# Performance work log

Measured on AMD Instinct MI355X. Metric: run time of the kernel, lower is better.

The kernel has to match this reference:

```python
import jax, jax.numpy as jnp
import numpy as np

EPS = 1e-5

@jax.custom_vjp
def binarize(x):
    # sign quantization: {-1, +1} (0 -> +1), as in BinaryNet Binarize
    return jnp.where(x >= 0, 1.0, -1.0).astype(x.dtype)

def _bin_fwd(x):
    return binarize(x), x

def _bin_bwd(res, g):
    # straight-through estimator with hardtanh clipping
    return (g * (jnp.abs(res) <= 1.0).astype(g.dtype),)

binarize.defvjp(_bin_fwd, _bin_bwd)


def batchnorm(x, gamma, beta):
    # BatchNorm1d, training mode: biased batch statistics over the batch axis
    mu = jnp.mean(x, axis=0)
    var = jnp.var(x, axis=0)
    return (x - mu) * jax.lax.rsqrt(var + EPS) * gamma + beta


def setup_inputs() -> dict:
    key = jax.random.key(0)
    ks = jax.random.split(key, 5)
    B, IND, HID, OUT = 16384, 768, 4096, 10
    return {
        "x": jax.random.normal(ks[0], (B, 784), jnp.float32),
        "w1": jax.random.normal(ks[1], (HID, IND), jnp.float32) * 0.05,
        "w2": jax.random.normal(ks[2], (HID, HID), jnp.float32) * 0.05,
        "w3": jax.random.normal(ks[3], (HID, HID), jnp.float32) * 0.05,
        "w4": jax.random.normal(ks[4], (OUT, HID), jnp.float32) * 0.05,
        "g1": jnp.ones(HID, jnp.float32), "b1": jnp.zeros(HID, jnp.float32),
        "g2": jnp.ones(HID, jnp.float32), "b2": jnp.zeros(HID, jnp.float32),
        "g3": jnp.ones(HID, jnp.float32), "b3": jnp.zeros(HID, jnp.float32),
        "g4": jnp.ones(OUT, jnp.float32), "b4": jnp.zeros(OUT, jnp.float32),
    }


def reference(x, w1, w2, w3, w4, g1, b1, g2, b2, g3, b3, g4, b4):
    # x.view(-1, 784); if width == 784, keep first 768 features
    h = x.reshape(-1, 784)[:, :768]
    # BinarizeLinear: binarize activations (width != 784) and weights, then matmul
    h = binarize(h) @ binarize(w1).T            # [B, 4096]
    h = jnp.clip(batchnorm(h, g1, b1), -1.0, 1.0)  # bn1 + hardtanh1
    h = binarize(h) @ binarize(w2).T
    h = jnp.clip(batchnorm(h, g2, b2), -1.0, 1.0)
    h = binarize(h) @ binarize(w3).T
    h = jnp.clip(batchnorm(h, g3, b3), -1.0, 1.0)
    h = binarize(h) @ binarize(w4).T            # [B, 10]
    h = batchnorm(h, g4, b4)
    return jax.nn.log_softmax(h, axis=1)
```

## Files before the change

### kernel.cpp

```cpp
#include <hip/hip_runtime.h>
#include <hip/hip_bf16.h>
#include <stdint.h>

typedef int v4i __attribute__((ext_vector_type(4)));

#define DEVI static __device__ __forceinline__

DEVI void gload16(const void* g, void* l) {
    __builtin_amdgcn_global_load_lds(
        (const __attribute__((address_space(1))) void*)g,
        (__attribute__((address_space(3))) void*)l,
        16, 0, 0);
}

#define WAITV(n) asm volatile("s_waitcnt vmcnt(" #n ")" ::: "memory")
#define SBAR()   __builtin_amdgcn_s_barrier()

__global__ __launch_bounds__(256) void k_bin_f32_to_i8(
    const float* __restrict__ w, int8_t* __restrict__ o, int n16)
{
    int t = blockIdx.x * 256 + threadIdx.x;
    if (t >= n16) return;
    const float4* s = (const float4*)w + (size_t)t * 4;
    union { int4 v; int8_t b[16]; } u;
#pragma unroll
    for (int i = 0; i < 4; ++i) {
        float4 f = s[i];
        u.b[i*4+0] = (f.x >= 0.f) ? (int8_t)1 : (int8_t)-1;
        u.b[i*4+1] = (f.y >= 0.f) ? (int8_t)1 : (int8_t)-1;
        u.b[i*4+2] = (f.z >= 0.f) ? (int8_t)1 : (int8_t)-1;
        u.b[i*4+3] = (f.w >= 0.f) ? (int8_t)1 : (int8_t)-1;
    }
    *(int4*)(o + (size_t)t * 16) = u.v;
}

__global__ __launch_bounds__(256) void k_bin_x(
    const float* __restrict__ x, int8_t* __restrict__ o)
{
    int t = blockIdx.x * 256 + threadIdx.x;
    int row = t / 48;
    int ch  = t % 48;
    const float4* s = (const float4*)(x + (size_t)row * 784 + ch * 16);
    union { int4 v; int8_t b[16]; } u;
#pragma unroll
    for (int i = 0; i < 4; ++i) {
        float4 f = s[i];
        u.b[i*4+0] = (f.x >= 0.f) ? (int8_t)1 : (int8_t)-1;
        u.b[i*4+1] = (f.y >= 0.f) ? (int8_t)1 : (int8_t)-1;
        u.b[i*4+2] = (f.z >= 0.f) ? (int8_t)1 : (int8_t)-1;
        u.b[i*4+3] = (f.w >= 0.f) ? (int8_t)1 : (int8_t)-1;
    }
    *(int4*)(o + (size_t)row * 768 + ch * 16) = u.v;
}

__global__ __launch_bounds__(512, 2)
void k_gemm256(const int8_t* __restrict__ A, const int8_t* __restrict__ B,
               int16_t* __restrict__ C, int* __restrict__ gsum,
               unsigned long long* __restrict__ gsq,
               int N, int K, int nbx)
{
    __shared__ __align__(16) int8_t lds[131072];

    const int tid  = threadIdx.x;
    const int lane = tid & 63;
    const int wave = tid >> 6;

    const int cpx = gridDim.x >> 3;
    const int id  = blockIdx.x;
    const int sw  = (id & 7) * cpx + (id >> 3);
    const int bx  = sw % nbx;
    const int by  = sw / nbx;

    const int NT = K >> 6;

    const int sr  = tid >> 2;
    const int asw = (((tid & 3) ^ ((sr >> 1) & 3)) << 4);
    const int8_t* gA0 = A + (size_t)(by * 256 + sr)       * K + asw;
    const int8_t* gA1 = A + (size_t)(by * 256 + 128 + sr) * K + asw;
    const int8_t* gB0 = B + (size_t)(bx * 256 + sr)       * K + asw;
    const int8_t* gB1 = B + (size_t)(bx * 256 + 128 + sr) * K + asw;
    const int ld0 = (wave * 64) << 4;
    const int ld1 = (512 + wave * 64) << 4;

    const int lrow = lane & 15;
    const int ksl  = lane >> 4;
    const int wr = (wave >> 2) * 128;
    const int wc = (wave & 3) * 64;
    const int fsw = ((ksl ^ ((lrow >> 1) & 3)) << 4);
    int aoff[8], boff[4];
#pragma unroll
    for (int m = 0; m < 8; ++m) aoff[m] = ((wr + m * 16 + lrow) << 6) + fsw;
#pragma unroll
    for (int n = 0; n < 4; ++n) boff[n] = ((wc + n * 16 + lrow) << 6) + fsw;

    v4i acc[8][4];
    v4i zero = {0, 0, 0, 0};
#pragma unroll
    for (int m = 0; m < 8; ++m)
#pragma unroll
        for (int n = 0; n < 4; ++n) acc[m][n] = zero;

#define STAGE_A(kt) do { const int _o = (kt) << 6; const int _b = ((kt) & 3) * 16384; \
        gload16(gA0 + _o, lds + _b + ld0); gload16(gA1 + _o, lds + _b + ld1); } while (0)
#define STAGE_B(kt) do { const int _o = (kt) << 6; const int _b = ((kt) & 3) * 16384; \
        gload16(gB0 + _o, lds + 65536 + _b + ld0); gload16(gB1 + _o, lds + 65536 + _b + ld1); } while (0)

#define READF(da, db, slot) do {                                                  \
        const int8_t* _ab = lds + ((slot) * 16384);                               \
        const int8_t* _bb = lds + 65536 + ((slot) * 16384);                       \
        _Pragma("unroll") for (int m = 0; m < 4; ++m)                             \
            da[m] = *(const v4i*)(_ab + aoff[m]);                                 \
        _Pragma("unroll") for (int n = 0; n < 4; ++n)                             \
            db[n] = *(const v4i*)(_bb + boff[n]); } while (0)

#define TILEF(kt, CA, CB, NA, NB) do {                                            \
        const int8_t* _ab = lds + (((kt) & 3) * 16384);                           \
        if ((kt) + 3 < NT) STAGE_A((kt) + 3);                                     \
        v4i _ag[4];                                                               \
        _Pragma("unroll") for (int m = 0; m < 4; ++m)                             \
            _ag[m] = *(const v4i*)(_ab + aoff[4 + m]);                            \
        SBAR();                                                                   \
        __builtin_amdgcn_s_setprio(1);                                            \
        _Pragma("unroll") for (int m = 0; m < 4; ++m)                             \
        _Pragma("unroll") for (int n = 0; n < 4; ++n)                             \
            acc[m][n] = __builtin_amdgcn_mfma_i32_16x16x64_i8(                    \
                CA[m], CB[n], acc[m][n], 0, 0, 0);                                \
        __builtin_amdgcn_s_setprio(0);                                            \
        SBAR();                                                                   \
        if ((kt) + 3 < NT) STAGE_B((kt) + 3);                                     \
        if ((kt) < NT - 3)       { WAITV(4); }                                    \
        else if ((kt) == NT - 3) { WAITV(0); }                                    \
        READF(NA, NB, ((kt) + 1) & 3);                                            \
        SBAR();                                                                   \
        __builtin_amdgcn_s_setprio(1);                                            \
        _Pragma("unroll") for (int m = 0; m < 4; ++m)                             \
        _Pragma("unroll") for (int n = 0; n < 4; ++n)                             \
            acc[4 + m][n] = __builtin_amdgcn_mfma_i32_16x16x64_i8(                \
                _ag[m], CB[n], acc[4 + m][n], 0, 0, 0);                           \
        __builtin_amdgcn_s_setprio(0);                                            \
        SBAR(); } while (0)

    STAGE_A(0); STAGE_B(0);
    STAGE_A(1); STAGE_B(1);
    STAGE_A(2); STAGE_B(2);
    WAITV(4);
    SBAR();

    v4i aX[4], bX[4], aY[4], bY[4];
    READF(aX, bX, 0);

    for (int kt = 0; kt < NT - 2; kt += 2) {
        TILEF(kt,     aX, bX, aY, bY);
        TILEF(kt + 1, aY, bY, aX, bX);
    }
    TILEF(NT - 2, aX, bX, aY, bY);
    {
        const int8_t* _ab = lds + (((NT - 1) & 3) * 16384);
        v4i ag[4];
#pragma unroll
        for (int m = 0; m < 4; ++m) ag[m] = *(const v4i*)(_ab + aoff[4 + m]);
        __builtin_amdgcn_s_setprio(1);
#pragma unroll
        for (int m = 0; m < 4; ++m)
#pragma unroll
            for (int n = 0; n < 4; ++n)
                acc[m][n] = __builtin_amdgcn_mfma_i32_16x16x64_i8(
                    aY[m], bY[n], acc[m][n], 0, 0, 0);
#pragma unroll
        for (int m = 0; m < 4; ++m)
#pragma unroll
            for (int n = 0; n < 4; ++n)
                acc[4 + m][n] = __builtin_amdgcn_mfma_i32_16x16x64_i8(
                    ag[m], bY[n], acc[4 + m][n], 0, 0, 0);
        __builtin_amdgcn_s_setprio(0);
    }
#undef STAGE_A
#undef STAGE_B
#undef READF
#undef TILEF

    const int row0 = by * 256 + wr + ksl * 4;
    const int col0 = bx * 256 + wc + lrow;
#pragma unroll
    for (int m = 0; m < 8; ++m)
#pragma unroll
        for (int rr = 0; rr < 4; ++rr) {
            int16_t* dst = C + (size_t)(row0 + m * 16 + rr) * N + col0;
#pragma unroll
            for (int n = 0; n < 4; ++n)
                dst[n * 16] = (int16_t)acc[m][n][rr];
        }
#pragma unroll
    for (int n = 0; n < 4; ++n) {
        int s = 0; unsigned q = 0;
#pragma unroll
        for (int m = 0; m < 8; ++m)
#pragma unroll
            for (int rr = 0; rr < 4; ++rr) {
                int v = acc[m][n][rr];
                s += v;
                q += (unsigned)(v * v);
            }
        s += __shfl_xor(s, 16);
        s += __shfl_xor(s, 32);
        q += (unsigned)__shfl_xor((int)q, 16);
        q += (unsigned)__shfl_xor((int)q, 32);
        if (ksl == 0) {
            const int col = col0 + n * 16;
            atomicAdd(&gsum[col], s);
            atomicAdd(&gsq[col], (unsigned long long)q);
        }
    }
}

__global__ __launch_bounds__(256)
void k_gemm4(const int8_t* __restrict__ A, const int8_t* __restrict__ Bw,
             int* __restrict__ C4, int K)
{
    const int lane = threadIdx.x & 63;
    const int wave = threadIdx.x >> 6;
    const int lrow = lane & 15, ksl = lane >> 4;
    const int r0 = blockIdx.x * 128 + wave * 32;
    const int k0 = blockIdx.y * 512;

    const int8_t* ap0 = A + (size_t)(r0 + lrow) * K + k0 + ksl * 16;
    const int8_t* ap1 = ap0 + (size_t)16 * K;
    const int8_t* bp  = Bw + (size_t)lrow * K + k0 + ksl * 16;

    v4i acc0 = {0,0,0,0}, acc1 = {0,0,0,0};
#pragma unroll
    for (int kk = 0; kk < 8; ++kk) {
        v4i a0 = *(const v4i*)(ap0 + kk * 64);
        v4i a1 = *(const v4i*)(ap1 + kk * 64);
        v4i b  = *(const v4i*)(bp  + kk * 64);
        acc0 = __builtin_amdgcn_mfma_i32_16x16x64_i8(a0, b, acc0, 0, 0, 0);
        acc1 = __builtin_amdgcn_mfma_i32_16x16x64_i8(a1, b, acc1, 0, 0, 0);
    }
#pragma unroll
    for (int rr = 0; rr < 4; ++rr) {
        atomicAdd(&C4[(size_t)(r0 + ksl * 4 + rr) * 16 + lrow], acc0[rr]);
        atomicAdd(&C4[(size_t)(r0 + 16 + ksl * 4 + rr) * 16 + lrow], acc1[rr]);
    }
}

__global__ __launch_bounds__(256)
void k_colstats4(const int* __restrict__ C4, int rows,
                 int* __restrict__ gsum, unsigned long long* __restrict__ gsq)
{
    const int col = threadIdx.x & 15, grp = threadIdx.x >> 4;
    const int rpb = rows / gridDim.x;
    const int r0  = blockIdx.x * rpb;
    int s = 0; unsigned long long q = 0;
    for (int r = grp; r < rpb; r += 16) {
        int v = C4[(size_t)(r0 + r) * 16 + col];
        s += v;
        q += (unsigned long long)((long long)v * (long long)v);
    }
    __shared__ int ss[256];
    __shared__ unsigned long long sq[256];
    ss[threadIdx.x] = s; sq[threadIdx.x] = q;
    __syncthreads();
    if (grp == 0) {
#pragma unroll
        for (int t = 1; t < 16; ++t) { s += ss[t * 16 + col]; q += sq[t * 16 + col]; }
        atomicAdd(&gsum[col], s);
        atomicAdd(&gsq[col], q);
    }
}

__global__ __launch_bounds__(128)
void k_finalize(const int* __restrict__ gsum, const unsigned long long* __restrict__ gsq,
                const float* __restrict__ gamma, const float* __restrict__ beta,
                float* __restrict__ pa, float* __restrict__ pb,
                int rows, int ncols_act, int ncols_pad)
{
    int c = blockIdx.x * 128 + threadIdx.x;
    if (c >= ncols_pad) return;
    double mu  = (double)gsum[c] / (double)rows;
    double var = (double)(long long)gsq[c] / (double)rows - mu * mu;
    float rs = rsqrtf((float)var + 1e-5f);
    float g  = (c < ncols_act) ? gamma[c] : 0.f;
    float be = (c < ncols_act) ? beta[c]  : 0.f;
    pa[c] = rs * g;
    pb[c] = be - (float)mu * rs * g;
}

__global__ __launch_bounds__(256)
void k_bnbin(const int16_t* __restrict__ C, const float* __restrict__ pa,
             const float* __restrict__ pb, int8_t* __restrict__ Aout,
             int n16, int colmask)
{
    int t = blockIdx.x * 256 + threadIdx.x;
    if (t >= n16) return;
    const size_t base = (size_t)t * 16;
    const int c0 = (int)(base & (size_t)colmask);
    union { int4 v; short s[8]; } u0, u1;
    u0.v = *(const int4*)(C + base);
    u1.v = *(const int4*)(C + base + 8);
    float4 a[4], b[4];
#pragma unroll
    for (int i = 0; i < 4; ++i) {
        a[i] = *(const float4*)(pa + c0 + i * 4);
        b[i] = *(const float4*)(pb + c0 + i * 4);
    }
    union { int4 v; int8_t b[16]; } o;
#pragma unroll
    for (int i = 0; i < 16; ++i) {
        float y = (float)((i < 8) ? u0.s[i] : u1.s[i - 8]);
        float aa = ((const float*)&a[i >> 2])[i & 3];
        float bb = ((const float*)&b[i >> 2])[i & 3];
        o.b[i] = (y * aa + bb >= 0.f) ? (int8_t)1 : (int8_t)-1;
    }
    *(int4*)(Aout + base) = o.v;
}

__global__ __launch_bounds__(256)
void k_logsoftmax(const int* __restrict__ C4, const float* __restrict__ pa,
                  const float* __restrict__ pb, float* __restrict__ out, int rows)
{
    int r = blockIdx.x * 256 + threadIdx.x;
    if (r >= rows) return;
    const int* row = C4 + (size_t)r * 16;
    float v[10];
    float m = -1e30f;
#pragma unroll
    for (int c = 0; c < 10; ++c) {
        v[c] = (float)row[c] * pa[c] + pb[c];
        m = fmaxf(m, v[c]);
    }
    float s = 0.f;
#pragma unroll
    for (int c = 0; c < 10; ++c) s += expf(v[c] - m);
    float ls = logf(s);
#pragma unroll
    for (int c = 0; c < 10; ++c) out[(size_t)r * 10 + c] = v[c] - m - ls;
}

extern "C" void kernel_launch(void* const* d_in, const int* in_sizes, int n_in,
                              void* d_out, int out_size, void* d_ws, size_t ws_size,
                              hipStream_t stream)
{
    (void)in_sizes; (void)n_in; (void)out_size; (void)ws_size;
    const float* x  = (const float*)d_in[0];
    const float* w1 = (const float*)d_in[1];
    const float* w2 = (const float*)d_in[2];
    const float* w3 = (const float*)d_in[3];
    const float* w4 = (const float*)d_in[4];
    const float* g1 = (const float*)d_in[5];
    const float* b1 = (const float*)d_in[6];
    const float* g2 = (const float*)d_in[7];
    const float* b2 = (const float*)d_in[8];
    const float* g3 = (const float*)d_in[9];
    const float* b3 = (const float*)d_in[10];
    const float* g4 = (const float*)d_in[11];
    const float* b4 = (const float*)d_in[12];
    float* out = (float*)d_out;

    const int B = 16384, HID = 4096, IND = 768;

    char* p = (char*)d_ws;
    size_t off = 0;
    auto alloc = [&](size_t sz) -> char* {
        char* r = p + off;
        off += (sz + 255) & ~(size_t)255;
        return r;
    };
    int8_t*  W1   = (int8_t*)alloc((size_t)HID * IND);
    int8_t*  W2   = (int8_t*)alloc((size_t)HID * HID);
    int8_t*  W3   = (int8_t*)alloc((size_t)HID * HID);
    int8_t*  W4p  = (int8_t*)alloc((size_t)16 * HID);
    int8_t*  Abuf = (int8_t*)alloc((size_t)B * HID);
    int16_t* C    = (int16_t*)alloc((size_t)B * HID * 2);
    int*     C4   = (int*)alloc((size_t)B * 16 * 4);
    int*     gsum = (int*)alloc((size_t)HID * 4);
    unsigned long long* gsq = (unsigned long long*)alloc((size_t)HID * 8);
    float*   pa   = (float*)alloc((size_t)HID * 4);
    float*   pb   = (float*)alloc((size_t)HID * 4);

    hipMemsetAsync(W4p, 0, (size_t)16 * HID, stream);
    k_bin_f32_to_i8<<<(HID * IND / 16 + 255) / 256, 256, 0, stream>>>(w1, W1, HID * IND / 16);
    k_bin_f32_to_i8<<<(HID * HID / 16 + 255) / 256, 256, 0, stream>>>(w2, W2, HID * HID / 16);
    k_bin_f32_to_i8<<<(HID * HID / 16 + 255) / 256, 256, 0, stream>>>(w3, W3, HID * HID / 16);
    k_bin_f32_to_i8<<<(10 * HID / 16 + 255) / 256, 256, 0, stream>>>(w4, W4p, 10 * HID / 16);
    k_bin_x<<<B * 48 / 256, 256, 0, stream>>>(x, Abuf);

    const int nbx = HID / 256, nby = B / 256;

    hipMemsetAsync(gsum, 0, HID * 12, stream);
    k_gemm256<<<nbx * nby, 512, 0, stream>>>(Abuf, W1, C, gsum, gsq, HID, IND, nbx);
    k_finalize<<<HID / 128, 128, 0, stream>>>(gsum, gsq, g1, b1, pa, pb, B, HID, HID);
    k_bnbin<<<B * HID / 16 / 256, 256, 0, stream>>>(C, pa, pb, Abuf, B * HID / 16, HID - 1);

    hipMemsetAsync(gsum, 0, HID * 12, stream);
    k_gemm256<<<nbx * nby, 512, 0, stream>>>(Abuf, W2, C, gsum, gsq, HID, HID, nbx);
    k_finalize<<<HID / 128, 128, 0, stream>>>(gsum, gsq, g2, b2, pa, pb, B, HID, HID);
    k_bnbin<<<B * HID / 16 / 256, 256, 0, stream>>>(C, pa, pb, Abuf, B * HID / 16, HID - 1);

    hipMemsetAsync(gsum, 0, HID * 12, stream);
    k_gemm256<<<nbx * nby, 512, 0, stream>>>(Abuf, W3, C, gsum, gsq, HID, HID, nbx);
    k_finalize<<<HID / 128, 128, 0, stream>>>(gsum, gsq, g3, b3, pa, pb, B, HID, HID);
    k_bnbin<<<B * HID / 16 / 256, 256, 0, stream>>>(C, pa, pb, Abuf, B * HID / 16, HID - 1);

    hipMemsetAsync(C4, 0, (size_t)B * 16 * 4, stream);
    k_gemm4<<<dim3(B / 128, 8), 256, 0, stream>>>(Abuf, W4p, C4, HID);
    hipMemsetAsync(gsum, 0, HID * 12, stream);
    k_colstats4<<<16, 256, 0, stream>>>(C4, B, gsum, gsq);
    k_finalize<<<1, 128, 0, stream>>>(gsum, gsq, g4, b4, pa, pb, B, 10, 16);
    k_logsoftmax<<<B / 256, 256, 0, stream>>>(C4, pa, pb, out, B);
}
```

Baseline: 803.8 us.

## Switch int8 GEMM to 32x32x32 MFMA and simplify per-tile pipeline barriers

```diff
diff --git a/kernel.cpp b/kernel.cpp
--- a/kernel.cpp
+++ b/kernel.cpp
@@ -2,7 +2,8 @@
 #include <hip/hip_bf16.h>
 #include <stdint.h>
 
-typedef int v4i __attribute__((ext_vector_type(4)));
+typedef int v4i  __attribute__((ext_vector_type(4)));
+typedef int v16i __attribute__((ext_vector_type(16)));
 
 #define DEVI static __device__ __forceinline__
 
@@ -80,63 +81,66 @@
     const int8_t* gB0 = B + (size_t)(bx * 256 + sr)       * K + asw;
     const int8_t* gB1 = B + (size_t)(bx * 256 + 128 + sr) * K + asw;
     const int ld0 = (wave * 64) << 4;
-    const int ld1 = (512 + wave * 64) << 4;
-
-    const int lrow = lane & 15;
-    const int ksl  = lane >> 4;
-    const int wr = (wave >> 2) * 128;
-    const int wc = (wave & 3) * 64;
-    const int fsw = ((ksl ^ ((lrow >> 1) & 3)) << 4);
-    int aoff[8], boff[4];
-#pragma unroll
-    for (int m = 0; m < 8; ++m) aoff[m] = ((wr + m * 16 + lrow) << 6) + fsw;
-#pragma unroll
-    for (int n = 0; n < 4; ++n) boff[n] = ((wc + n * 16 + lrow) << 6) + fsw;
-
-    v4i acc[8][4];
-    v4i zero = {0, 0, 0, 0};
-#pragma unroll
-    for (int m = 0; m < 8; ++m)
-#pragma unroll
-        for (int n = 0; n < 4; ++n) acc[m][n] = zero;
+    const int ld1 = ld0 + 8192;
+
+    const int lrow = lane & 31;
+    const int ksl  = lane >> 5;
+    const int wr  = (wave >> 2) * 128;
+    const int wc  = (wave & 3) * 64;
+    const int key = (lrow >> 1) & 3;
+    int aoff[2][4], boff[2][2];
+#pragma unroll
+    for (int s = 0; s < 2; ++s) {
+        const int fs = ((s * 2 + ksl) ^ key) << 4;
+#pragma unroll
+        for (int m = 0; m < 4; ++m) aoff[s][m] = ((wr + m * 32 + lrow) << 6) + fs;
+#pragma unroll
+        for (int n = 0; n < 2; ++n) boff[s][n] = ((wc + n * 32 + lrow) << 6) + fs;
+    }
+
+    v16i acc[4][2];
+#pragma unroll
+    for (int m = 0; m < 4; ++m)
+#pragma unroll
+        for (int n = 0; n < 2; ++n)
+#pragma unroll
+            for (int r = 0; r < 16; ++r) acc[m][n][r] = 0;
 
 #define STAGE_A(kt) do { const int _o = (kt) << 6; const int _b = ((kt) & 3) * 16384; \
         gload16(gA0 + _o, lds + _b + ld0); gload16(gA1 + _o, lds + _b + ld1); } while (0)
 #define STAGE_B(kt) do { const int _o = (kt) << 6; const int _b = ((kt) & 3) * 16384; \
         gload16(gB0 + _o, lds + 65536 + _b + ld0); gload16(gB1 + _o, lds + 65536 + _b + ld1); } while (0)
 
-#define READF(da, db, slot) do {                                                  \
-        const int8_t* _ab = lds + ((slot) * 16384);                               \
-        const int8_t* _bb = lds + 65536 + ((slot) * 16384);                       \
+#define TILE(kt, CA, CB, NA, NB) do {                                             \
+        const int8_t* _ab = lds + (((kt) & 3) * 16384);                           \
+        const int8_t* _bb = lds + 65536 + (((kt) & 3) * 16384);                   \
+        if ((kt) + 3 < NT) { STAGE_A((kt) + 3); STAGE_B((kt) + 3); }              \
+        if ((kt) < NT - 3)       { WAITV(4); }                                    \
+        else if ((kt) == NT - 3) { WAITV(0); }                                    \
+        v4i _ag[4], _bg[2];                                                       \
         _Pragma("unroll") for (int m = 0; m < 4; ++m)                             \
-            da[m] = *(const v4i*)(_ab + aoff[m]);                                 \
-        _Pragma("unroll") for (int n = 0; n < 4; ++n)                             \
-            db[n] = *(const v4i*)(_bb + boff[n]); } while (0)
-
-#define TILEF(kt, CA, CB, NA, NB) do {                                            \
-        const int8_t* _ab = lds + (((kt) & 3) * 16384);                           \
-        if ((kt) + 3 < NT) STAGE_A((kt) + 3);                                     \
-        v4i _ag[4];                                                               \
-        _Pragma("unroll") for (int m = 0; m < 4; ++m)                             \
-            _ag[m] = *(const v4i*)(_ab + aoff[4 + m]);                            \
-        SBAR();                                                                   \
+            _ag[m] = *(const v4i*)(_ab + aoff[1][m]);                             \
+        _Pragma("unroll") for (int n = 0; n < 2; ++n)                             \
+            _bg[n] = *(const v4i*)(_bb + boff[1][n]);                             \
         __builtin_amdgcn_s_setprio(1);                                            \
         _Pragma("unroll") for (int m = 0; m < 4; ++m)                             \
-        _Pragma("unroll") for (int n = 0; n < 4; ++n)                             \
-            acc[m][n] = __builtin_amdgcn_mfma_i32_16x16x64_i8(                    \
+        _Pragma("unroll") for (int n = 0; n < 2; ++n)                             \
+            acc[m][n] = __builtin_amdgcn_mfma_i32_32x32x32_i8(                    \
                 CA[m], CB[n], acc[m][n], 0, 0, 0);                                \
         __builtin_amdgcn_s_setprio(0);                                            \
-        SBAR();                                                                   \
-        if ((kt) + 3 < NT) STAGE_B((kt) + 3);                                     \
-        if ((kt) < NT - 3)       { WAITV(4); }                                    \
-        else if ((kt) == NT - 3) { WAITV(0); }                                    \
-        READF(NA, NB, ((kt) + 1) & 3);                                            \
-        SBAR();                                                                   \
+        if ((kt) + 1 < NT) {                                                      \
+            const int8_t* _abN = lds + ((((kt) + 1) & 3) * 16384);                \
+            const int8_t* _bbN = lds + 65536 + ((((kt) + 1) & 3) * 16384);        \
+            _Pragma("unroll") for (int m = 0; m < 4; ++m)                         \
+                NA[m] = *(const v4i*)(_abN + aoff[0][m]);                         \
+            _Pragma("unroll") for (int n = 0; n < 2; ++n)                         \
+                NB[n] = *(const v4i*)(_bbN + boff[0][n]);                         \
+        }                                                                         \
         __builtin_amdgcn_s_setprio(1);                                            \
         _Pragma("unroll") for (int m = 0; m < 4; ++m)                             \
-        _Pragma("unroll") for (int n = 0; n < 4; ++n)                             \
-            acc[4 + m][n] = __builtin_amdgcn_mfma_i32_16x16x64_i8(                \
-                _ag[m], CB[n], acc[4 + m][n], 0, 0, 0);                           \
+        _Pragma("unroll") for (int n = 0; n < 2; ++n)                             \
+            acc[m][n] = __builtin_amdgcn_mfma_i32_32x32x32_i8(                    \
+                _ag[m], _bg[n], acc[m][n], 0, 0, 0);                              \
         __builtin_amdgcn_s_setprio(0);                                            \
         SBAR(); } while (0)
 
@@ -146,67 +150,49 @@
     WAITV(4);
     SBAR();
 
-    v4i aX[4], bX[4], aY[4], bY[4];
-    READF(aX, bX, 0);
-
-    for (int kt = 0; kt < NT - 2; kt += 2) {
-        TILEF(kt,     aX, bX, aY, bY);
-        TILEF(kt + 1, aY, bY, aX, bX);
-    }
-    TILEF(NT - 2, aX, bX, aY, bY);
+    v4i aX[4], bX[2], aY[4], bY[2];
     {
-        const int8_t* _ab = lds + (((NT - 1) & 3) * 16384);
-        v4i ag[4];
-#pragma unroll
-        for (int m = 0; m < 4; ++m) ag[m] = *(const v4i*)(_ab + aoff[4 + m]);
-        __builtin_amdgcn_s_setprio(1);
-#pragma unroll
-        for (int m = 0; m < 4; ++m)
-#pragma unroll
-            for (int n = 0; n < 4; ++n)
-                acc[m][n] = __builtin_amdgcn_mfma_i32_16x16x64_i8(
-                    aY[m], bY[n], acc[m][n], 0, 0, 0);
-#pragma unroll
-        for (int m = 0; m < 4; ++m)
-#pragma unroll
-            for (int n = 0; n < 4; ++n)
-                acc[4 + m][n] = __builtin_amdgcn_mfma_i32_16x16x64_i8(
-                    ag[m], bY[n], acc[4 + m][n], 0, 0, 0);
-        __builtin_amdgcn_s_setprio(0);
+        const int8_t* ab = lds;
+        const int8_t* bb = lds + 65536;
+#pragma unroll
+        for (int m = 0; m < 4; ++m) aX[m] = *(const v4i*)(ab + aoff[0][m]);
+#pragma unroll
+        for (int n = 0; n < 2; ++n) bX[n] = *(const v4i*)(bb + boff[0][n]);
+    }
+
+    for (int kt = 0; kt < NT; kt += 2) {
+        TILE(kt,     aX, bX, aY, bY);
+        TILE(kt + 1, aY, bY, aX, bX);
     }
 #undef STAGE_A
 #undef STAGE_B
-#undef READF
-#undef TILEF
-
-    const int row0 = by * 256 + wr + ksl * 4;
+#undef TILE
+
     const int col0 = bx * 256 + wc + lrow;
 #pragma unroll
-    for (int m = 0; m < 8; ++m)
-#pragma unroll
-        for (int rr = 0; rr < 4; ++rr) {
-            int16_t* dst = C + (size_t)(row0 + m * 16 + rr) * N + col0;
-#pragma unroll
-            for (int n = 0; n < 4; ++n)
-                dst[n * 16] = (int16_t)acc[m][n][rr];
+    for (int m = 0; m < 4; ++m)
+#pragma unroll
+        for (int r = 0; r < 16; ++r) {
+            const int row = by * 256 + wr + m * 32 + (r & 3) + 8 * (r >> 2) + 4 * ksl;
+            int16_t* dst = C + (size_t)row * N + col0;
+            dst[0]  = (int16_t)acc[m][0][r];
+            dst[32] = (int16_t)acc[m][1][r];
         }
 #pragma unroll
-    for (int n = 0; n < 4; ++n) {
+    for (int n = 0; n < 2; ++n) {
         int s = 0; unsigned q = 0;
 #pragma unroll
-        for (int m = 0; m < 8; ++m)
-#pragma unroll
-            for (int rr = 0; rr < 4; ++rr) {
-                int v = acc[m][n][rr];
+        for (int m = 0; m < 4; ++m)
+#pragma unroll
+            for (int r = 0; r < 16; ++r) {
+                int v = acc[m][n][r];
                 s += v;
                 q += (unsigned)(v * v);
             }
-        s += __shfl_xor(s, 16);
         s += __shfl_xor(s, 32);
-        q += (unsigned)__shfl_xor((int)q, 16);
         q += (unsigned)__shfl_xor((int)q, 32);
         if (ksl == 0) {
-            const int col = col0 + n * 16;
+            const int col = col0 + n * 32;
             atomicAdd(&gsum[col], s);
             atomicAdd(&gsq[col], (unsigned long long)q);
         }
```

After: 823.7 us. 1.02x slower.
